# Kernel optimization log

Hardware: AMD Instinct MI355X
Metric: run time of the kernel (lower is better)

The kernel has to match this reference:

```python
import jax, jax.numpy as jnp
import numpy as np

T, D, E, K = 8192, 4096, 64, 8


def setup_inputs() -> dict:
    key = jax.random.key(0)
    k1, k2, k3, k4 = jax.random.split(key, 4)
    x = jax.random.normal(k1, (T, D), dtype=jnp.float32)
    # nn.Linear stores weight as [out_features, in_features]
    Wg = jax.random.normal(k2, (E, D), dtype=jnp.float32) * (1.0 / np.sqrt(D))
    Wc = jax.random.normal(k3, (E, D), dtype=jnp.float32) * (1.0 / np.sqrt(D))
    extra_scale = jnp.zeros((E,), dtype=jnp.float32)  # init zeros as in module
    extra_bias = jax.random.normal(k4, (E,), dtype=jnp.float32) * 0.01
    return {"x": x, "Wg": Wg, "Wc": Wc, "extra_scale": extra_scale,
            "extra_bias": extra_bias, "topk": K}


def reference(x, Wg, Wc, extra_scale, extra_bias, topk):
    # scores = |classifier(x) * silu(gate(x))|, softmax in fp32
    gate = jnp.einsum('td,ed->te', x, Wg)        # [T, E]
    cls = jnp.einsum('td,ed->te', x, Wc)         # [T, E]
    scores = jnp.abs(cls * jax.nn.silu(gate))
    scores = jax.nn.softmax(scores.astype(jnp.float32), axis=-1)
    biased = scores + extra_bias[None, :]        # load-balance bias, used only for selection
    _, indices = jax.lax.top_k(biased, topk)     # [T, K]
    original = 1.0 + scores * extra_scale[None, :]
    weights = jnp.take_along_axis(original, indices, axis=1)  # [T, K]
    return weights.astype(x.dtype), indices
```

## Files before the change

### kernel.cpp

```cpp
#include <hip/hip_runtime.h>
#include <math.h>


#define T_DIM 8192
#define D_DIM 4096
#define E_DIM 64
#define N2    128
#define KTOP  8
#define MB_ROWS 128

typedef __attribute__((ext_vector_type(8)))  short bfrag8;
typedef __attribute__((ext_vector_type(16))) float f32x16;

__device__ __forceinline__ unsigned short f2bf_rne(float f) {
    unsigned int u = __float_as_uint(f);
    unsigned int r = u + 0x7fffu + ((u >> 16) & 1u);
    return (unsigned short)(r >> 16);
}
__device__ __forceinline__ float bf2f(unsigned short h) {
    return __uint_as_float(((unsigned int)h) << 16);
}
__device__ __forceinline__ void split3(float v, unsigned short& h,
                                       unsigned short& m, unsigned short& l) {
    h = f2bf_rne(v);
    const float r1 = v - bf2f(h);
    m = f2bf_rne(r1);
    const float r2 = r1 - bf2f(m);
    l = f2bf_rne(r2);
}

__device__ __forceinline__ void gload16(const void* g, void* l) {
    __builtin_amdgcn_global_load_lds(
        (const __attribute__((address_space(1))) void*)g,
        (__attribute__((address_space(3))) void*)l, 16, 0, 0);
}

__global__ __launch_bounds__(256)
void router_prep(const float* __restrict__ Wg, const float* __restrict__ Wc,
                 unsigned short* __restrict__ Wpk)
{
    const int t   = blockIdx.x * 256 + threadIdx.x;
    const int col = t >> 9;
    const int ch  = t & 511;
    const int k   = ch << 3;

    const float* src = (col < E_DIM) ? (Wg + (size_t)col * D_DIM)
                                     : (Wc + (size_t)(col - E_DIM) * D_DIM);
    const float4 w0 = ((const float4*)(src + k))[0];
    const float4 w1 = ((const float4*)(src + k))[1];
    const float v[8] = {w0.x, w0.y, w0.z, w0.w, w1.x, w1.y, w1.z, w1.w};

    unsigned short hv[8], mv[8], lv[8];
    #pragma unroll
    for (int j = 0; j < 8; ++j) split3(v[j], hv[j], mv[j], lv[j]);

    const int k32 = k >> 5, h2 = (k >> 4) & 1, lh = (k >> 3) & 1;
    const int n = col >> 5, lane = lh * 32 + (col & 31);
    const size_t base = ((((size_t)k32 * 4 + n) * 3 + 0) * 2 + h2) * 512 + (size_t)lane * 8;
    *(ushort4*)(Wpk + base)          = make_ushort4(hv[0], hv[1], hv[2], hv[3]);
    *(ushort4*)(Wpk + base + 4)      = make_ushort4(hv[4], hv[5], hv[6], hv[7]);
    *(ushort4*)(Wpk + base + 1024)   = make_ushort4(mv[0], mv[1], mv[2], mv[3]);
    *(ushort4*)(Wpk + base + 1028)   = make_ushort4(mv[4], mv[5], mv[6], mv[7]);
    *(ushort4*)(Wpk + base + 2048)   = make_ushort4(lv[0], lv[1], lv[2], lv[3]);
    *(ushort4*)(Wpk + base + 2052)   = make_ushort4(lv[4], lv[5], lv[6], lv[7]);
}

__global__ __launch_bounds__(256, 2)
void router_gemm(const float* __restrict__ x,
                 const unsigned short* __restrict__ Wpk,
                 float* __restrict__ P,
                 int sliceK)
{
    __shared__ float sA[2][MB_ROWS * 32];

    const int tid  = threadIdx.x;
    const int lane = tid & 63;
    const int wid  = tid >> 6;
    const int l31  = lane & 31;
    const int lh   = lane >> 5;
    const int mb   = blockIdx.x;
    const int ks   = blockIdx.y;
    const int k0   = ks * sliceK;
    const int NT   = sliceK >> 5;
    const int brow0 = mb * MB_ROWS;
    const int rl   = wid * 32 + l31;
    const int sw   = l31 & 7;

    f32x16 acc[4];
    #pragma unroll
    for (int n = 0; n < 4; ++n)
        #pragma unroll
        for (int r = 0; r < 16; ++r)
            acc[n][r] = 0.f;

    #define STAGE(bf_, kk_)                                                      \
        {                                                                        \
            _Pragma("unroll")                                                    \
            for (int i_ = 0; i_ < 4; ++i_) {                                     \
                const int chunk_ = i_ * 256 + tid;                               \
                const int row_   = chunk_ >> 3;                                  \
                const int csrc_  = (chunk_ & 7) ^ (row_ & 7);                    \
                const float* gp_ = x + (size_t)(brow0 + row_) * D_DIM            \
                                     + (kk_) + csrc_ * 4;                        \
                gload16(gp_, &sA[bf_][chunk_ * 4]);                              \
            }                                                                    \
        }

    STAGE(0, k0);
    __syncthreads();

    for (int t = 0; t < NT; ++t) {
        const int kk = k0 + t * 32;
        const int bf = t & 1;

        if (t + 1 < NT) STAGE(bf ^ 1, kk + 32);

        bfrag8 ah[2], am[2], al[2];
        #pragma unroll
        for (int h2 = 0; h2 < 2; ++h2) {
            const int c0 = h2 * 4 + lh * 2;
            const float4 q0 = *(const float4*)&sA[bf][rl * 32 + ((c0    ) ^ sw) * 4];
            const float4 q1 = *(const float4*)&sA[bf][rl * 32 + ((c0 + 1) ^ sw) * 4];
            const float f[8] = {q0.x, q0.y, q0.z, q0.w, q1.x, q1.y, q1.z, q1.w};
            #pragma unroll
            for (int j = 0; j < 8; ++j) {
                unsigned short h, m, l;
                split3(f[j], h, m, l);
                ah[h2][j] = (short)h; am[h2][j] = (short)m; al[h2][j] = (short)l;
            }
        }

        const size_t k32 = (size_t)(kk >> 5);
        #pragma unroll
        for (int n = 0; n < 4; ++n) {
            #pragma unroll
            for (int h2 = 0; h2 < 2; ++h2) {
                const unsigned short* bb =
                    Wpk + ((((k32 * 4 + n) * 3 + 0) * 2 + h2) * 64 + lane) * 8;
                const bfrag8 bh = *(const bfrag8*)(bb);
                const bfrag8 bm = *(const bfrag8*)(bb + 1024);
                const bfrag8 bl = *(const bfrag8*)(bb + 2048);
                acc[n] = __builtin_amdgcn_mfma_f32_32x32x16_bf16(ah[h2], bl, acc[n], 0, 0, 0);
                acc[n] = __builtin_amdgcn_mfma_f32_32x32x16_bf16(al[h2], bh, acc[n], 0, 0, 0);
                acc[n] = __builtin_amdgcn_mfma_f32_32x32x16_bf16(am[h2], bm, acc[n], 0, 0, 0);
                acc[n] = __builtin_amdgcn_mfma_f32_32x32x16_bf16(ah[h2], bm, acc[n], 0, 0, 0);
                acc[n] = __builtin_amdgcn_mfma_f32_32x32x16_bf16(am[h2], bh, acc[n], 0, 0, 0);
                acc[n] = __builtin_amdgcn_mfma_f32_32x32x16_bf16(ah[h2], bh, acc[n], 0, 0, 0);
            }
        }

        __syncthreads();
    }

    float* Pb = P + ((size_t)ks * T_DIM + brow0 + wid * 32) * N2 + l31;
    #pragma unroll
    for (int n = 0; n < 4; ++n)
        #pragma unroll
        for (int r = 0; r < 16; ++r) {
            const int wrow = (r & 3) + 8 * (r >> 2) + 4 * lh;
            Pb[(size_t)wrow * N2 + n * 32] = acc[n][r];
        }
}

__global__ __launch_bounds__(256)
void router_topk(const float* __restrict__ P,
                 const float* __restrict__ scale,
                 const float* __restrict__ bias,
                 float* __restrict__ out,
                 int ksplit)
{
    const int lane = threadIdx.x & 63;
    const int wid  = threadIdx.x >> 6;
    const int row  = blockIdx.x * 4 + wid;

    float g = 0.f, c = 0.f;
    for (int ks = 0; ks < ksplit; ++ks) {
        const float* p = P + ((size_t)ks * T_DIM + row) * N2;
        g += p[lane];
        c += p[E_DIM + lane];
    }
    const float sg = g / (1.f + expf(-g));
    const float v  = fabsf(c * sg);

    float m = v;
    #pragma unroll
    for (int off = 32; off >= 1; off >>= 1) m = fmaxf(m, __shfl_xor(m, off));
    const float e = expf(v - m);
    float Z = e;
    #pragma unroll
    for (int off = 32; off >= 1; off >>= 1) Z += __shfl_xor(Z, off);
    const float s = e / Z;

    const float sc  = scale[lane];
    float cur = s + bias[lane];

    float myw = 0.f; int myi = 0;
    #pragma unroll
    for (int j = 0; j < KTOP; ++j) {
        float bv = cur; int bi = lane;
        #pragma unroll
        for (int off = 32; off >= 1; off >>= 1) {
            const float ov = __shfl_xor(bv, off);
            const int   oi = __shfl_xor(bi, off);
            if (ov > bv || (ov == bv && oi < bi)) { bv = ov; bi = oi; }
        }
        const float s_bi  = __shfl(s,  bi);
        const float sc_bi = __shfl(sc, bi);
        const float w = 1.f + s_bi * sc_bi;
        if (lane == j)  { myw = w; myi = bi; }
        if (lane == bi) cur = -INFINITY;
    }

    if (lane < KTOP) {
        out[(size_t)row * KTOP + lane] = myw;
        out[(size_t)T_DIM * KTOP + (size_t)row * KTOP + lane] = (float)myi;
    }
}

extern "C" void kernel_launch(void* const* d_in, const int* in_sizes, int n_in,
                              void* d_out, int out_size, void* d_ws, size_t ws_size,
                              hipStream_t stream)
{
    const float* x  = (const float*)d_in[0];
    const float* Wg = (const float*)d_in[1];
    const float* Wc = (const float*)d_in[2];
    const float* sc = (const float*)d_in[3];
    const float* bs = (const float*)d_in[4];
    float* out = (float*)d_out;
    float* P   = (float*)d_ws;

    const size_t PER = (size_t)T_DIM * N2 * sizeof(float);
    const size_t WSP = (size_t)N2 * D_DIM * sizeof(unsigned short);

    int S = 8;
    while (S > 1 && (size_t)S * PER + 3 * WSP > ws_size) S >>= 1;
    const int sliceK = D_DIM / S;

    unsigned short* Wpk = (unsigned short*)((char*)d_ws + (size_t)S * PER);

    router_prep<<<256, 256, 0, stream>>>(Wg, Wc, Wpk);
    router_gemm<<<dim3(T_DIM / MB_ROWS, S), 256, 0, stream>>>(x, Wpk, P, sliceK);
    router_topk<<<T_DIM / 4, 256, 0, stream>>>(P, sc, bs, out, S);
}
```

Baseline: 298.4 us.

## Split router GEMM output columns across 8 waves with 64-row tiles

Each block now handles 64 rows with 512 threads arranged as 2 row-waves by 4 column-waves, so each wave owns a single 32x32 accumulator instead of four. This cuts per-wave accumulator registers and raises occupancy and block count, aiming to better hide the latency of staging x and loading weights. The trade-off is that each wave now splits its own A fragment into three bf16 parts, and four waves redo this split for the same rows, so the conversion work per block goes up. Global traffic for W also rises because every block reads the full W slice for half as many rows.

Result: faster. 278.3 us (-6.8%).

```diff
diff --git a/kernel.cpp b/kernel.cpp
--- a/kernel.cpp
+++ b/kernel.cpp
@@ -7,7 +7,7 @@
 #define E_DIM 64
 #define N2    128
 #define KTOP  8
-#define MB_ROWS 128
+#define MB_ROWS 64
 
 typedef __attribute__((ext_vector_type(8)))  short bfrag8;
 typedef __attribute__((ext_vector_type(16))) float f32x16;
@@ -65,7 +65,7 @@
     *(ushort4*)(Wpk + base + 2052)   = make_ushort4(lv[4], lv[5], lv[6], lv[7]);
 }
 
-__global__ __launch_bounds__(256, 2)
+__global__ __launch_bounds__(512, 4)
 void router_gemm(const float* __restrict__ x,
                  const unsigned short* __restrict__ Wpk,
                  float* __restrict__ P,
@@ -76,6 +76,8 @@
     const int tid  = threadIdx.x;
     const int lane = tid & 63;
     const int wid  = tid >> 6;
+    const int wr   = wid >> 2;
+    const int wc   = wid & 3;
     const int l31  = lane & 31;
     const int lh   = lane >> 5;
     const int mb   = blockIdx.x;
@@ -83,27 +85,21 @@
     const int k0   = ks * sliceK;
     const int NT   = sliceK >> 5;
     const int brow0 = mb * MB_ROWS;
-    const int rl   = wid * 32 + l31;
+    const int rl   = wr * 32 + l31;
     const int sw   = l31 & 7;
 
-    f32x16 acc[4];
-    #pragma unroll
-    for (int n = 0; n < 4; ++n)
-        #pragma unroll
-        for (int r = 0; r < 16; ++r)
-            acc[n][r] = 0.f;
+    f32x16 acc;
+    #pragma unroll
+    for (int r = 0; r < 16; ++r) acc[r] = 0.f;
 
     #define STAGE(bf_, kk_)                                                      \
         {                                                                        \
-            _Pragma("unroll")                                                    \
-            for (int i_ = 0; i_ < 4; ++i_) {                                     \
-                const int chunk_ = i_ * 256 + tid;                               \
-                const int row_   = chunk_ >> 3;                                  \
-                const int csrc_  = (chunk_ & 7) ^ (row_ & 7);                    \
-                const float* gp_ = x + (size_t)(brow0 + row_) * D_DIM            \
-                                     + (kk_) + csrc_ * 4;                        \
-                gload16(gp_, &sA[bf_][chunk_ * 4]);                              \
-            }                                                                    \
+            const int chunk_ = tid;                                              \
+            const int row_   = chunk_ >> 3;                                      \
+            const int csrc_  = (chunk_ & 7) ^ (row_ & 7);                        \
+            const float* gp_ = x + (size_t)(brow0 + row_) * D_DIM                \
+                                 + (kk_) + csrc_ * 4;                            \
+            gload16(gp_, &sA[bf_][chunk_ * 4]);                                  \
         }
 
     STAGE(0, k0);
@@ -132,34 +128,30 @@
 
         const size_t k32 = (size_t)(kk >> 5);
         #pragma unroll
-        for (int n = 0; n < 4; ++n) {
-            #pragma unroll
-            for (int h2 = 0; h2 < 2; ++h2) {
-                const unsigned short* bb =
-                    Wpk + ((((k32 * 4 + n) * 3 + 0) * 2 + h2) * 64 + lane) * 8;
-                const bfrag8 bh = *(const bfrag8*)(bb);
-                const bfrag8 bm = *(const bfrag8*)(bb + 1024);
-                const bfrag8 bl = *(const bfrag8*)(bb + 2048);
-                acc[n] = __builtin_amdgcn_mfma_f32_32x32x16_bf16(ah[h2], bl, acc[n], 0, 0, 0);
-                acc[n] = __builtin_amdgcn_mfma_f32_32x32x16_bf16(al[h2], bh, acc[n], 0, 0, 0);
-                acc[n] = __builtin_amdgcn_mfma_f32_32x32x16_bf16(am[h2], bm, acc[n], 0, 0, 0);
-                acc[n] = __builtin_amdgcn_mfma_f32_32x32x16_bf16(ah[h2], bm, acc[n], 0, 0, 0);
-                acc[n] = __builtin_amdgcn_mfma_f32_32x32x16_bf16(am[h2], bh, acc[n], 0, 0, 0);
-                acc[n] = __builtin_amdgcn_mfma_f32_32x32x16_bf16(ah[h2], bh, acc[n], 0, 0, 0);
-            }
+        for (int h2 = 0; h2 < 2; ++h2) {
+            const unsigned short* bb =
+                Wpk + ((((k32 * 4 + wc) * 3 + 0) * 2 + h2) * 64 + lane) * 8;
+            const bfrag8 bh = *(const bfrag8*)(bb);
+            const bfrag8 bm = *(const bfrag8*)(bb + 1024);
+            const bfrag8 bl = *(const bfrag8*)(bb + 2048);
+            acc = __builtin_amdgcn_mfma_f32_32x32x16_bf16(ah[h2], bl, acc, 0, 0, 0);
+            acc = __builtin_amdgcn_mfma_f32_32x32x16_bf16(al[h2], bh, acc, 0, 0, 0);
+            acc = __builtin_amdgcn_mfma_f32_32x32x16_bf16(am[h2], bm, acc, 0, 0, 0);
+            acc = __builtin_amdgcn_mfma_f32_32x32x16_bf16(ah[h2], bm, acc, 0, 0, 0);
+            acc = __builtin_amdgcn_mfma_f32_32x32x16_bf16(am[h2], bh, acc, 0, 0, 0);
+            acc = __builtin_amdgcn_mfma_f32_32x32x16_bf16(ah[h2], bh, acc, 0, 0, 0);
         }
 
         __syncthreads();
     }
 
-    float* Pb = P + ((size_t)ks * T_DIM + brow0 + wid * 32) * N2 + l31;
-    #pragma unroll
-    for (int n = 0; n < 4; ++n)
-        #pragma unroll
-        for (int r = 0; r < 16; ++r) {
-            const int wrow = (r & 3) + 8 * (r >> 2) + 4 * lh;
-            Pb[(size_t)wrow * N2 + n * 32] = acc[n][r];
-        }
+    float* Pb = P + ((size_t)ks * T_DIM + brow0 + wr * 32) * N2 + wc * 32 + l31;
+    #pragma unroll
+    for (int r = 0; r < 16; ++r) {
+        const int wrow = (r & 3) + 8 * (r >> 2) + 4 * lh;
+        Pb[(size_t)wrow * N2] = acc[r];
+    }
+    #undef STAGE
 }
 
 __global__ __launch_bounds__(256)
@@ -239,6 +231,6 @@
     unsigned short* Wpk = (unsigned short*)((char*)d_ws + (size_t)S * PER);
 
     router_prep<<<256, 256, 0, stream>>>(Wg, Wc, Wpk);
-    router_gemm<<<dim3(T_DIM / MB_ROWS, S), 256, 0, stream>>>(x, Wpk, P, sliceK);
+    router_gemm<<<dim3(T_DIM / MB_ROWS, S), 512, 0, stream>>>(x, Wpk, P, sliceK);
     router_topk<<<T_DIM / 4, 256, 0, stream>>>(P, sc, bs, out, S);
 }
```
